# Kernel optimization log

Measured on AMD Instinct MI355X. Metric: run time of the kernel, lower is better.

Reference implementation:

```python
import jax, jax.numpy as jnp
import numpy as np

B = 65536
QUERY_DIM = 1024
CROSS_DIM = 1024
HEADS = 16
DIM_HEAD = 64
INNER = HEADS * DIM_HEAD  # 1024
SCALE = DIM_HEAD ** -0.5


def setup_inputs() -> dict:
    key = jax.random.key(0)
    ks = jax.random.split(key, 7)
    s_in = 1.0 / np.sqrt(QUERY_DIM)
    s_c = 1.0 / np.sqrt(CROSS_DIM)
    s_o = 1.0 / np.sqrt(INNER)
    return {
        "latent": jax.random.normal(ks[0], (B, QUERY_DIM), jnp.float32),
        "cond_latent": jax.random.normal(ks[1], (B, CROSS_DIM), jnp.float32),
        "Wq": jax.random.normal(ks[2], (INNER, QUERY_DIM), jnp.float32) * s_in,
        "Wk": jax.random.normal(ks[3], (INNER, CROSS_DIM), jnp.float32) * s_c,
        "Wv": jax.random.normal(ks[4], (INNER, CROSS_DIM), jnp.float32) * s_c,
        "Wout": jax.random.normal(ks[5], (QUERY_DIM, INNER), jnp.float32) * s_o,
        "bout": jax.random.normal(ks[6], (QUERY_DIM,), jnp.float32) * s_o,
    }


def reference(latent, cond_latent, Wq, Wk, Wv, Wout, bout):
    # projections: [B, inner] -> [B, heads, dim_head]
    Q = (latent @ Wq.T).reshape(B, HEADS, DIM_HEAD)
    K = (cond_latent @ Wk.T).reshape(B, HEADS, DIM_HEAD)
    V = (cond_latent @ Wv.T).reshape(B, HEADS, DIM_HEAD)
    # attention across the heads axis: scores [B, heads, heads]
    scores = jnp.einsum("bhd,bgd->bhg", Q, K) * SCALE
    probs = jax.nn.softmax(scores, axis=-1)
    feats = jnp.einsum("bhg,bgd->bhd", probs, V).reshape(B, INNER)
    return feats @ Wout.T + bout
```

## Files before the change

kernel.cpp:

```cpp
#include <hip/hip_runtime.h>
#include <hip/hip_bf16.h>

#define NB    65536
#define KDIM  1024
#define NDIM  1024

#define BM 256
#define BN 256
#define BK 32
#define NT (KDIM / BK)

typedef float f32x4  __attribute__((ext_vector_type(4)));
typedef short short8 __attribute__((ext_vector_type(8)));
typedef unsigned short ushort8v __attribute__((ext_vector_type(8)));

static __device__ __forceinline__ unsigned short f2bf(float f) {
    union { float f; unsigned u; } v; v.f = f;
    unsigned r = v.u + 0x7FFFu + ((v.u >> 16) & 1u);
    return (unsigned short)(r >> 16);
}
static __device__ __forceinline__ float bf2f(unsigned short h) {
    union { unsigned u; float f; } v; v.u = ((unsigned)h) << 16;
    return v.f;
}

static __device__ __forceinline__ void gload16(const unsigned short* g, unsigned short* l) {
    __builtin_amdgcn_global_load_lds(
        (const __attribute__((address_space(1))) unsigned int*)g,
        (__attribute__((address_space(3))) unsigned int*)l, 16, 0, 0);
}


__global__ __launch_bounds__(256) void pack_f32_k(
    const float* __restrict__ src, unsigned short* __restrict__ dst)
{
    const int tid = threadIdx.x;
    const int r   = blockIdx.x * 16 + (tid >> 4);
    const int cb  = (tid & 15) * 64;
    const int p   = r >> 8;
    const int f   = (r >> 4) & 15;
    const int rl  = r & 15;
    const float* s = src + (size_t)r * 1024 + cb;
#pragma unroll
    for (int g = 0; g < 8; ++g) {
        float4 va = *reinterpret_cast<const float4*>(s + g * 8);
        float4 vb = *reinterpret_cast<const float4*>(s + g * 8 + 4);
        ushort8v o;
        o[0] = f2bf(va.x); o[1] = f2bf(va.y); o[2] = f2bf(va.z); o[3] = f2bf(va.w);
        o[4] = f2bf(vb.x); o[5] = f2bf(vb.y); o[6] = f2bf(vb.z); o[7] = f2bf(vb.w);
        const int c0 = cb + g * 8;
        const int t  = c0 >> 5;
        const int kc = (c0 & 31) >> 3;
        *reinterpret_cast<ushort8v*>(
            &dst[((size_t)(p * 32 + t) * 16 + f) * 512 + kc * 128 + rl * 8]) = o;
    }
}

template<int OUT_F32, int NN>
__global__ __launch_bounds__(512, 2) void gemm256(
    const unsigned short* __restrict__ Ap, const unsigned short* __restrict__ Wp,
    const float* __restrict__ bias, void* __restrict__ Cptr)
{
    constexpr int GN = NN / BN;
    __shared__ alignas(16) unsigned short lds[4][2][16][512];

    const int t    = threadIdx.x;
    const int lane = t & 63;
    const int wid  = t >> 6;
    const int wm   = wid >> 2;
    const int wn   = wid & 3;

    const int nwg  = gridDim.x;
    const int cpx  = nwg >> 3;
    const int orig = blockIdx.x;
    const int wgid = (orig & 7) * cpx + (orig >> 3);
    const int bn0  = (wgid & (GN - 1)) * BN;
    const int bm0  = (wgid / GN) * BM;

    const int pA = bm0 >> 8;
    const int pB = bn0 >> 8;

#define STAGE_(TAU, SLOT) do {                                                  \
        int _tc = (TAU) < NT ? (TAU) : NT - 1;                                  \
        _Pragma("unroll")                                                       \
        for (int _ab = 0; _ab < 2; ++_ab) {                                     \
            const unsigned short* _b = _ab ? Wp : Ap;                           \
            int _pp = _ab ? pB : pA;                                            \
            _Pragma("unroll")                                                   \
            for (int _j = 0; _j < 2; ++_j) {                                    \
                int _f = wid * 2 + _j;                                          \
                gload16(_b + ((size_t)(_pp * 32 + _tc) * 16 + _f) * 512 + lane * 8, \
                        &lds[SLOT][_ab][_f][0]);                                \
            }                                                                   \
        }                                                                       \
    } while (0)

    f32x4 acc[8][4];
#pragma unroll
    for (int mi = 0; mi < 8; ++mi)
#pragma unroll
        for (int ni = 0; ni < 4; ++ni)
            acc[mi][ni] = (f32x4){0.f, 0.f, 0.f, 0.f};

    STAGE_(0, 0); STAGE_(1, 1); STAGE_(2, 2);

#pragma unroll 1
    for (int tt = 0; tt < NT; ++tt) {
        const int slot = tt & 3;
        STAGE_(tt + 3, (tt + 3) & 3);
        asm volatile("s_waitcnt vmcnt(12)" ::: "memory");
        __builtin_amdgcn_s_barrier();

        short8 af[8], bq[4];
#pragma unroll
        for (int mi = 0; mi < 8; ++mi)
            af[mi] = *reinterpret_cast<const short8*>(&lds[slot][0][wm * 8 + mi][lane * 8]);
#pragma unroll
        for (int ni = 0; ni < 4; ++ni)
            bq[ni] = *reinterpret_cast<const short8*>(&lds[slot][1][wn * 4 + ni][lane * 8]);
        __builtin_amdgcn_s_setprio(1);
#pragma unroll
        for (int mi = 0; mi < 8; ++mi)
#pragma unroll
            for (int ni = 0; ni < 4; ++ni)
                acc[mi][ni] = __builtin_amdgcn_mfma_f32_16x16x32_bf16(
                    af[mi], bq[ni], acc[mi][ni], 0, 0, 0);
        __builtin_amdgcn_s_setprio(0);
        __builtin_amdgcn_s_barrier();
    }
    asm volatile("s_waitcnt vmcnt(0)" ::: "memory");
    __builtin_amdgcn_s_barrier();

    const int crow = (lane >> 4) * 4;
    const int ccol = lane & 15;
    if (OUT_F32) {
        float* Cf = (float*)Cptr;
        float* bbf = reinterpret_cast<float*>(&lds[0][0][0][0]);
        float bv[4];
#pragma unroll
        for (int ni = 0; ni < 4; ++ni)
            bv[ni] = bias[bn0 + wn * 64 + ni * 16 + ccol];
#pragma unroll
        for (int p = 0; p < 4; ++p) {
            if (wm == (p >> 1)) {
#pragma unroll
                for (int ml = 0; ml < 4; ++ml)
#pragma unroll
                    for (int ni = 0; ni < 4; ++ni)
#pragma unroll
                        for (int r = 0; r < 4; ++r)
                            bbf[(ml * 16 + crow + r) * 268 + wn * 64 + ni * 16 + ccol]
                                = acc[(p & 1) * 4 + ml][ni][r] + bv[ni];
            }
            __syncthreads();
#pragma unroll
            for (int it = 0; it < 8; ++it) {
                int lrow = wid * 8 + it;
                f32x4 v = *reinterpret_cast<const f32x4*>(&bbf[lrow * 268 + lane * 4]);
                *reinterpret_cast<f32x4*>(
                    &Cf[(size_t)(bm0 + p * 64 + lrow) * NN + bn0 + lane * 4]) = v;
            }
            __syncthreads();
        }
    } else {
        unsigned short* Cb = (unsigned short*)Cptr;
        unsigned short* bb = &lds[0][0][0][0];
#pragma unroll
        for (int p = 0; p < 2; ++p) {
            if (wm == p) {
#pragma unroll
                for (int ml = 0; ml < 8; ++ml)
#pragma unroll
                    for (int ni = 0; ni < 4; ++ni)
#pragma unroll
                        for (int r = 0; r < 4; ++r)
                            bb[(ml * 16 + crow + r) * 264 + wn * 64 + ni * 16 + ccol]
                                = f2bf(acc[ml][ni][r]);
            }
            __syncthreads();
#pragma unroll
            for (int it = 0; it < 8; ++it) {
                int lrow = wid * 16 + it * 2 + (lane >> 5);
                int lcol = (lane & 31) * 8;
                ushort8v v = *reinterpret_cast<const ushort8v*>(&bb[lrow * 264 + lcol]);
                *reinterpret_cast<ushort8v*>(
                    &Cb[(size_t)(bm0 + p * 128 + lrow) * NN + bn0 + lcol]) = v;
            }
            __syncthreads();
        }
    }
#undef STAGE_
}

__global__ __launch_bounds__(1024) void attn_k(
    const unsigned short* __restrict__ Qb, const unsigned short* __restrict__ KVb,
    unsigned short* __restrict__ Fp)
{
    __shared__ alignas(16) unsigned short KL[16][1024];
    __shared__ alignas(16) unsigned short VL[16][1024];
    const int t = threadIdx.x;
    const int lane = t & 63;
    const int wid = t >> 6;
    const size_t row = (size_t)blockIdx.x * 16 + wid;
    const size_t base = row * 1024;
    const size_t bkv  = row * 2048;
    const int off = lane * 16;

    ushort8v q0 = *reinterpret_cast<const ushort8v*>(&Qb[base + off]);
    ushort8v q1 = *reinterpret_cast<const ushort8v*>(&Qb[base + off + 8]);
    float qf[16];
#pragma unroll
    for (int j = 0; j < 8; ++j) { qf[j] = bf2f(q0[j]); qf[8 + j] = bf2f(q1[j]); }

    *reinterpret_cast<ushort8v*>(&KL[wid][off])     = *reinterpret_cast<const ushort8v*>(&KVb[bkv + off]);
    *reinterpret_cast<ushort8v*>(&KL[wid][off + 8]) = *reinterpret_cast<const ushort8v*>(&KVb[bkv + off + 8]);
    *reinterpret_cast<ushort8v*>(&VL[wid][off])     = *reinterpret_cast<const ushort8v*>(&KVb[bkv + 1024 + off]);
    *reinterpret_cast<ushort8v*>(&VL[wid][off + 8]) = *reinterpret_cast<const ushort8v*>(&KVb[bkv + 1024 + off + 8]);
    __syncthreads();

    const int sub = lane & 3;
    float s[16];
#pragma unroll
    for (int g = 0; g < 16; ++g) {
        const ushort8v k0 = *reinterpret_cast<const ushort8v*>(&KL[wid][g * 64 + sub * 16]);
        const ushort8v k1 = *reinterpret_cast<const ushort8v*>(&KL[wid][g * 64 + sub * 16 + 8]);
        float acc = 0.f;
#pragma unroll
        for (int j = 0; j < 8; ++j)
            acc += qf[j] * bf2f(k0[j]) + qf[8 + j] * bf2f(k1[j]);
        s[g] = acc;
    }
#pragma unroll
    for (int m = 1; m <= 2; m <<= 1)
#pragma unroll
        for (int g = 0; g < 16; ++g)
            s[g] += __shfl_xor(s[g], m, 64);

    float mx = s[0];
#pragma unroll
    for (int g = 1; g < 16; ++g) mx = fmaxf(mx, s[g]);
    float p[16], denom = 0.f;
#pragma unroll
    for (int g = 0; g < 16; ++g) {
        p[g] = __expf((s[g] - mx) * 0.125f);
        denom += p[g];
    }
    float inv = 1.f / denom;

    float f[16];
#pragma unroll
    for (int j = 0; j < 16; ++j) f[j] = 0.f;
#pragma unroll
    for (int g = 0; g < 16; ++g) {
        float pg = p[g] * inv;
        const ushort8v v0 = *reinterpret_cast<const ushort8v*>(&VL[wid][g * 64 + sub * 16]);
        const ushort8v v1 = *reinterpret_cast<const ushort8v*>(&VL[wid][g * 64 + sub * 16 + 8]);
#pragma unroll
        for (int j = 0; j < 8; ++j) {
            f[j]     += pg * bf2f(v0[j]);
            f[8 + j] += pg * bf2f(v1[j]);
        }
    }
    ushort8v o0, o1;
#pragma unroll
    for (int j = 0; j < 8; ++j) { o0[j] = f2bf(f[j]); o1[j] = f2bf(f[8 + j]); }
    *reinterpret_cast<ushort8v*>(&KL[wid][off])     = o0;
    *reinterpret_cast<ushort8v*>(&KL[wid][off + 8]) = o1;
    __syncthreads();

    const int r0 = blockIdx.x * 16;
    const int pp = r0 >> 8;
    const int ff = (r0 >> 4) & 15;
    const int tt = t >> 5;
    const int kc = (t >> 3) & 3;
    const int rp = t & 7;
    unsigned short* db = &Fp[((size_t)(pp * 32 + tt) * 16 + ff) * 512 + kc * 128 + rp * 16];
    *reinterpret_cast<ushort8v*>(db)     = *reinterpret_cast<const ushort8v*>(&KL[rp * 2][tt * 32 + kc * 8]);
    *reinterpret_cast<ushort8v*>(db + 8) = *reinterpret_cast<const ushort8v*>(&KL[rp * 2 + 1][tt * 32 + kc * 8]);
}

extern "C" void kernel_launch(void* const* d_in, const int* in_sizes, int n_in,
                              void* d_out, int out_size, void* d_ws, size_t ws_size,
                              hipStream_t stream)
{
    (void)in_sizes; (void)n_in; (void)out_size; (void)ws_size;
    const float* latent = (const float*)d_in[0];
    const float* cond   = (const float*)d_in[1];
    const float* Wq     = (const float*)d_in[2];
    const float* Wk     = (const float*)d_in[3];
    const float* Wv     = (const float*)d_in[4];
    const float* Wout   = (const float*)d_in[5];
    const float* bout   = (const float*)d_in[6];
    float* out = (float*)d_out;

    char* ws = (char*)d_ws;
    const size_t MB = 1ull << 20;
    unsigned short* wqp  = (unsigned short*)(ws + 0 * MB);
    unsigned short* wkvp = (unsigned short*)(ws + 2 * MB);
    unsigned short* wop  = (unsigned short*)(ws + 6 * MB);
    unsigned short* Qb   = (unsigned short*)(ws + 8 * MB);
    unsigned short* KVb  = (unsigned short*)(ws + 136 * MB);
    unsigned short* Lp   = (unsigned short*)(ws + 392 * MB);
    unsigned short* Cp   = (unsigned short*)(ws + 520 * MB);
    unsigned short* Fp   = Lp;

    pack_f32_k<<<NDIM / 16, 256, 0, stream>>>(Wq,   wqp);
    pack_f32_k<<<NDIM / 16, 256, 0, stream>>>(Wk,   wkvp);
    pack_f32_k<<<NDIM / 16, 256, 0, stream>>>(Wv,   wkvp + 1048576);
    pack_f32_k<<<NDIM / 16, 256, 0, stream>>>(Wout, wop);

    pack_f32_k<<<NB / 16, 256, 0, stream>>>(latent, Lp);
    pack_f32_k<<<NB / 16, 256, 0, stream>>>(cond,   Cp);

    gemm256<0, 1024><<<1024, 512, 0, stream>>>(Lp, wqp,  nullptr, Qb);
    gemm256<0, 2048><<<2048, 512, 0, stream>>>(Cp, wkvp, nullptr, KVb);

    attn_k<<<NB / 16, 1024, 0, stream>>>(Qb, KVb, Fp);

    gemm256<1, 1024><<<1024, 512, 0, stream>>>(Fp, wop, bout, out);
}
```

Before: 1.013 ms.

## Split GEMM K-loop into two half-phases interleaving LDS reads, global prefetch and MFMA

Restructures the main GEMM loop into two phases per K-tile. Each phase reads half the A fragments from LDS, issues half of the next stage's global-to-LDS loads, waits, and then runs a 4x4 MFMA block. This is meant to overlap LDS reads and global load issue with matrix math and to lower register pressure from holding all eight A fragments at once. In exchange it adds barriers per iteration and depends on the reworked vmcnt accounting being correct.

```diff
diff --git a/kernel.cpp b/kernel.cpp
--- a/kernel.cpp
+++ b/kernel.cpp
@@ -80,21 +80,23 @@
     const int pA = bm0 >> 8;
     const int pB = bn0 >> 8;
 
-#define STAGE_(TAU, SLOT) do {                                                  \
+#define STAGE1_(TAU, SLOT, AB) do {                                             \
         int _tc = (TAU) < NT ? (TAU) : NT - 1;                                  \
+        const unsigned short* _b = (AB) ? Wp : Ap;                              \
+        int _pp = (AB) ? pB : pA;                                               \
         _Pragma("unroll")                                                       \
-        for (int _ab = 0; _ab < 2; ++_ab) {                                     \
-            const unsigned short* _b = _ab ? Wp : Ap;                           \
-            int _pp = _ab ? pB : pA;                                            \
-            _Pragma("unroll")                                                   \
-            for (int _j = 0; _j < 2; ++_j) {                                    \
-                int _f = wid * 2 + _j;                                          \
-                gload16(_b + ((size_t)(_pp * 32 + _tc) * 16 + _f) * 512 + lane * 8, \
-                        &lds[SLOT][_ab][_f][0]);                                \
-            }                                                                   \
+        for (int _j = 0; _j < 2; ++_j) {                                        \
+            int _f = wid * 2 + _j;                                              \
+            gload16(_b + ((size_t)(_pp * 32 + _tc) * 16 + _f) * 512 + lane * 8, \
+                    &lds[SLOT][AB][_f][0]);                                     \
         }                                                                       \
     } while (0)
 
+#define LDA_(S, MI) \
+    (*reinterpret_cast<const short8*>(&lds[S][0][wm * 8 + (MI)][lane * 8]))
+#define LDB_(S, NI) \
+    (*reinterpret_cast<const short8*>(&lds[S][1][wn * 4 + (NI)][lane * 8]))
+
     f32x4 acc[8][4];
 #pragma unroll
     for (int mi = 0; mi < 8; ++mi)
@@ -102,29 +104,47 @@
         for (int ni = 0; ni < 4; ++ni)
             acc[mi][ni] = (f32x4){0.f, 0.f, 0.f, 0.f};
 
-    STAGE_(0, 0); STAGE_(1, 1); STAGE_(2, 2);
+    STAGE1_(0, 0, 0); STAGE1_(0, 0, 1);
+    STAGE1_(1, 1, 0); STAGE1_(1, 1, 1);
+    STAGE1_(2, 2, 0); STAGE1_(2, 2, 1);
+    asm volatile("s_waitcnt vmcnt(8)" ::: "memory");
+    __builtin_amdgcn_s_barrier();
 
 #pragma unroll 1
     for (int tt = 0; tt < NT; ++tt) {
         const int slot = tt & 3;
-        STAGE_(tt + 3, (tt + 3) & 3);
-        asm volatile("s_waitcnt vmcnt(12)" ::: "memory");
+        short8 af0[4], af1[4], bq[4];
+
+#pragma unroll
+        for (int mi = 0; mi < 4; ++mi) af0[mi] = LDA_(slot, mi);
+#pragma unroll
+        for (int ni = 0; ni < 4; ++ni) bq[ni] = LDB_(slot, ni);
+        STAGE1_(tt + 3, (tt + 3) & 3, 0);
         __builtin_amdgcn_s_barrier();
-
-        short8 af[8], bq[4];
-#pragma unroll
-        for (int mi = 0; mi < 8; ++mi)
-            af[mi] = *reinterpret_cast<const short8*>(&lds[slot][0][wm * 8 + mi][lane * 8]);
-#pragma unroll
-        for (int ni = 0; ni < 4; ++ni)
-            bq[ni] = *reinterpret_cast<const short8*>(&lds[slot][1][wn * 4 + ni][lane * 8]);
+        asm volatile("s_waitcnt lgkmcnt(0)" ::: "memory");
         __builtin_amdgcn_s_setprio(1);
 #pragma unroll
-        for (int mi = 0; mi < 8; ++mi)
+        for (int mi = 0; mi < 4; ++mi)
 #pragma unroll
             for (int ni = 0; ni < 4; ++ni)
                 acc[mi][ni] = __builtin_amdgcn_mfma_f32_16x16x32_bf16(
-                    af[mi], bq[ni], acc[mi][ni], 0, 0, 0);
+                    af0[mi], bq[ni], acc[mi][ni], 0, 0, 0);
+        __builtin_amdgcn_s_setprio(0);
+        __builtin_amdgcn_s_barrier();
+
+#pragma unroll
+        for (int mi = 0; mi < 4; ++mi) af1[mi] = LDA_(slot, 4 + mi);
+        STAGE1_(tt + 3, (tt + 3) & 3, 1);
+        asm volatile("s_waitcnt vmcnt(8)" ::: "memory");
+        __builtin_amdgcn_s_barrier();
+        asm volatile("s_waitcnt lgkmcnt(0)" ::: "memory");
+        __builtin_amdgcn_s_setprio(1);
+#pragma unroll
+        for (int mi = 0; mi < 4; ++mi)
+#pragma unroll
+            for (int ni = 0; ni < 4; ++ni)
+                acc[4 + mi][ni] = __builtin_amdgcn_mfma_f32_16x16x32_bf16(
+                    af1[mi], bq[ni], acc[4 + mi][ni], 0, 0, 0);
         __builtin_amdgcn_s_setprio(0);
         __builtin_amdgcn_s_barrier();
     }
@@ -189,7 +209,9 @@
             __syncthreads();
         }
     }
-#undef STAGE_
+#undef STAGE1_
+#undef LDA_
+#undef LDB_
 }
 
 __global__ __launch_bounds__(1024) void attn_k(
```

New measurement: 1.005 ms. No clear change (-0.7%).

## Shrink GEMM tiles to 128x128 with 4 waves and double-buffered staging

Applied to the files above, without the earlier changes.

Replaces the 256x256, 8-wave GEMM with a 128x128, 4-wave kernel at higher occupancy, and swaps the 4-slot, 3-ahead prefetch for a 2-slot double buffer that waits for all loads at the end of each k-step. The epilogues are rewritten for the smaller tile. The intent is more workgroups and more waves per CU for latency hiding. In exchange, data reuse per tile is lower, global/LDS traffic per flop is higher, and each iteration's full vmcnt(0) wait leaves the pipeline shallower.

```diff
diff --git a/kernel.cpp b/kernel.cpp
--- a/kernel.cpp
+++ b/kernel.cpp
@@ -5,8 +5,8 @@
 #define KDIM  1024
 #define NDIM  1024
 
-#define BM 256
-#define BN 256
+#define BM 128
+#define BN 128
 #define BK 32
 #define NT (KDIM / BK)
 
@@ -57,18 +57,18 @@
 }
 
 template<int OUT_F32, int NN>
-__global__ __launch_bounds__(512, 2) void gemm256(
+__global__ __launch_bounds__(256, 4) void gemm128(
     const unsigned short* __restrict__ Ap, const unsigned short* __restrict__ Wp,
     const float* __restrict__ bias, void* __restrict__ Cptr)
 {
     constexpr int GN = NN / BN;
-    __shared__ alignas(16) unsigned short lds[4][2][16][512];
+    __shared__ alignas(16) unsigned short lds[2][2][8][512];
 
     const int t    = threadIdx.x;
     const int lane = t & 63;
     const int wid  = t >> 6;
-    const int wm   = wid >> 2;
-    const int wn   = wid & 3;
+    const int wm   = wid >> 1;
+    const int wn   = wid & 1;
 
     const int nwg  = gridDim.x;
     const int cpx  = nwg >> 3;
@@ -77,8 +77,8 @@
     const int bn0  = (wgid & (GN - 1)) * BN;
     const int bm0  = (wgid / GN) * BM;
 
-    const int pA = bm0 >> 8;
-    const int pB = bn0 >> 8;
+    const int pA  = bm0 >> 8;  const int f0A = (bm0 >> 4) & 15;
+    const int pB  = bn0 >> 8;  const int f0B = (bn0 >> 4) & 15;
 
 #define STAGE_(TAU, SLOT) do {                                                  \
         int _tc = (TAU) < NT ? (TAU) : NT - 1;                                  \
@@ -86,55 +86,56 @@
         for (int _ab = 0; _ab < 2; ++_ab) {                                     \
             const unsigned short* _b = _ab ? Wp : Ap;                           \
             int _pp = _ab ? pB : pA;                                            \
+            int _f0 = _ab ? f0B : f0A;                                          \
             _Pragma("unroll")                                                   \
             for (int _j = 0; _j < 2; ++_j) {                                    \
                 int _f = wid * 2 + _j;                                          \
-                gload16(_b + ((size_t)(_pp * 32 + _tc) * 16 + _f) * 512 + lane * 8, \
+                gload16(_b + ((size_t)(_pp * 32 + _tc) * 16 + _f0 + _f) * 512 + lane * 8, \
                         &lds[SLOT][_ab][_f][0]);                                \
             }                                                                   \
         }                                                                       \
     } while (0)
 
-    f32x4 acc[8][4];
-#pragma unroll
-    for (int mi = 0; mi < 8; ++mi)
+    f32x4 acc[4][4];
+#pragma unroll
+    for (int mi = 0; mi < 4; ++mi)
 #pragma unroll
         for (int ni = 0; ni < 4; ++ni)
             acc[mi][ni] = (f32x4){0.f, 0.f, 0.f, 0.f};
 
-    STAGE_(0, 0); STAGE_(1, 1); STAGE_(2, 2);
+    STAGE_(0, 0);
+    asm volatile("s_waitcnt vmcnt(0)" ::: "memory");
+    __builtin_amdgcn_s_barrier();
 
 #pragma unroll 1
     for (int tt = 0; tt < NT; ++tt) {
-        const int slot = tt & 3;
-        STAGE_(tt + 3, (tt + 3) & 3);
-        asm volatile("s_waitcnt vmcnt(12)" ::: "memory");
-        __builtin_amdgcn_s_barrier();
-
-        short8 af[8], bq[4];
-#pragma unroll
-        for (int mi = 0; mi < 8; ++mi)
-            af[mi] = *reinterpret_cast<const short8*>(&lds[slot][0][wm * 8 + mi][lane * 8]);
+        const int slot = tt & 1;
+        if (tt + 1 < NT) STAGE_(tt + 1, slot ^ 1);
+
+        short8 af[4], bq[4];
+#pragma unroll
+        for (int mi = 0; mi < 4; ++mi)
+            af[mi] = *reinterpret_cast<const short8*>(&lds[slot][0][wm * 4 + mi][lane * 8]);
 #pragma unroll
         for (int ni = 0; ni < 4; ++ni)
             bq[ni] = *reinterpret_cast<const short8*>(&lds[slot][1][wn * 4 + ni][lane * 8]);
         __builtin_amdgcn_s_setprio(1);
 #pragma unroll
-        for (int mi = 0; mi < 8; ++mi)
+        for (int mi = 0; mi < 4; ++mi)
 #pragma unroll
             for (int ni = 0; ni < 4; ++ni)
                 acc[mi][ni] = __builtin_amdgcn_mfma_f32_16x16x32_bf16(
                     af[mi], bq[ni], acc[mi][ni], 0, 0, 0);
         __builtin_amdgcn_s_setprio(0);
+        asm volatile("s_waitcnt vmcnt(0)" ::: "memory");
         __builtin_amdgcn_s_barrier();
     }
-    asm volatile("s_waitcnt vmcnt(0)" ::: "memory");
-    __builtin_amdgcn_s_barrier();
 
     const int crow = (lane >> 4) * 4;
     const int ccol = lane & 15;
+
     if (OUT_F32) {
-        float* Cf = (float*)Cptr;
+        float* Cf  = (float*)Cptr;
         float* bbf = reinterpret_cast<float*>(&lds[0][0][0][0]);
         float bv[4];
 #pragma unroll
@@ -144,21 +145,24 @@
         for (int p = 0; p < 4; ++p) {
             if (wm == (p >> 1)) {
 #pragma unroll
-                for (int ml = 0; ml < 4; ++ml)
+                for (int mlo = 0; mlo < 2; ++mlo) {
+                    int ml = (p & 1) * 2 + mlo;
 #pragma unroll
                     for (int ni = 0; ni < 4; ++ni)
 #pragma unroll
                         for (int r = 0; r < 4; ++r)
-                            bbf[(ml * 16 + crow + r) * 268 + wn * 64 + ni * 16 + ccol]
-                                = acc[(p & 1) * 4 + ml][ni][r] + bv[ni];
+                            bbf[(mlo * 16 + crow + r) * 136 + wn * 64 + ni * 16 + ccol]
+                                = acc[ml][ni][r] + bv[ni];
+                }
             }
             __syncthreads();
 #pragma unroll
-            for (int it = 0; it < 8; ++it) {
-                int lrow = wid * 8 + it;
-                f32x4 v = *reinterpret_cast<const f32x4*>(&bbf[lrow * 268 + lane * 4]);
+            for (int it = 0; it < 4; ++it) {
+                int lrow = it * 8 + (t >> 5);
+                int lcol = (t & 31) * 4;
+                f32x4 v = *reinterpret_cast<const f32x4*>(&bbf[lrow * 136 + lcol]);
                 *reinterpret_cast<f32x4*>(
-                    &Cf[(size_t)(bm0 + p * 64 + lrow) * NN + bn0 + lane * 4]) = v;
+                    &Cf[(size_t)(bm0 + p * 32 + lrow) * NN + bn0 + lcol]) = v;
             }
             __syncthreads();
         }
@@ -169,22 +173,22 @@
         for (int p = 0; p < 2; ++p) {
             if (wm == p) {
 #pragma unroll
-                for (int ml = 0; ml < 8; ++ml)
+                for (int ml = 0; ml < 4; ++ml)
 #pragma unroll
                     for (int ni = 0; ni < 4; ++ni)
 #pragma unroll
                         for (int r = 0; r < 4; ++r)
-                            bb[(ml * 16 + crow + r) * 264 + wn * 64 + ni * 16 + ccol]
+                            bb[(ml * 16 + crow + r) * 136 + wn * 64 + ni * 16 + ccol]
                                 = f2bf(acc[ml][ni][r]);
             }
             __syncthreads();
 #pragma unroll
-            for (int it = 0; it < 8; ++it) {
-                int lrow = wid * 16 + it * 2 + (lane >> 5);
-                int lcol = (lane & 31) * 8;
-                ushort8v v = *reinterpret_cast<const ushort8v*>(&bb[lrow * 264 + lcol]);
+            for (int it = 0; it < 4; ++it) {
+                int lrow = it * 16 + (t >> 4);
+                int lcol = (t & 15) * 8;
+                ushort8v v = *reinterpret_cast<const ushort8v*>(&bb[lrow * 136 + lcol]);
                 *reinterpret_cast<ushort8v*>(
-                    &Cb[(size_t)(bm0 + p * 128 + lrow) * NN + bn0 + lcol]) = v;
+                    &Cb[(size_t)(bm0 + p * 64 + lrow) * NN + bn0 + lcol]) = v;
             }
             __syncthreads();
         }
@@ -312,10 +316,10 @@
     pack_f32_k<<<NB / 16, 256, 0, stream>>>(latent, Lp);
     pack_f32_k<<<NB / 16, 256, 0, stream>>>(cond,   Cp);
 
-    gemm256<0, 1024><<<1024, 512, 0, stream>>>(Lp, wqp,  nullptr, Qb);
-    gemm256<0, 2048><<<2048, 512, 0, stream>>>(Cp, wkvp, nullptr, KVb);
+    gemm128<0, 1024><<<(NB / 128) * (1024 / 128), 256, 0, stream>>>(Lp, wqp,  nullptr, Qb);
+    gemm128<0, 2048><<<(NB / 128) * (2048 / 128), 256, 0, stream>>>(Cp, wkvp, nullptr, KVb);
 
     attn_k<<<NB / 16, 1024, 0, stream>>>(Qb, KVb, Fp);
 
-    gemm256<1, 1024><<<1024, 512, 0, stream>>>(Fp, wop, bout, out);
-}
+    gemm128<1, 1024><<<(NB / 128) * (1024 / 128), 256, 0, stream>>>(Fp, wop, bout, out);
+}
```

Measured after the change: 1.046 ms. 1.03x slower.
